# Optimization experiments

Measured on AMD Instinct MI355X. Metric: run time of the kernel, lower is better.

## Reference

```python
import jax, jax.numpy as jnp
import numpy as np

N_HEAD = 12
D_HEAD = 64


def setup_inputs() -> dict:
    key = jax.random.key(0)
    ks = jax.random.split(key, 9)
    bs, seq, d_model = 4, 2048, 768
    sc = 1.0 / np.sqrt(d_model)
    return {
        "q": jax.random.normal(ks[0], (bs, seq, d_model), jnp.float32),
        "k": jax.random.normal(ks[1], (bs, seq, d_model), jnp.float32),
        "v": jax.random.normal(ks[2], (bs, seq, d_model), jnp.float32),
        "Wq": jax.random.normal(ks[3], (d_model, d_model), jnp.float32) * sc,
        "bq": jax.random.normal(ks[4], (d_model,), jnp.float32) * 0.01,
        "Wk": jax.random.normal(ks[5], (d_model, d_model), jnp.float32) * sc,
        "bk": jax.random.normal(ks[6], (d_model,), jnp.float32) * 0.01,
        "Wv": jax.random.normal(ks[7], (d_model, d_model), jnp.float32) * sc,
        "bv": jax.random.normal(ks[8], (d_model,), jnp.float32) * 0.01,
    }


def _split_heads(x):
    # [bs, seq, n_head*d_head] -> [bs, n_head, seq, d_head]
    bs, seq, _ = x.shape
    return x.reshape(bs, seq, N_HEAD, D_HEAD).transpose(0, 2, 1, 3)


def reference(q, k, v, Wq, bq, Wk, bk, Wv, bv):
    # Linear projections (torch Linear: x @ W.T + b)
    wq = _split_heads(q @ Wq.T + bq)
    wk = _split_heads(k @ Wk.T + bk)
    wv = _split_heads(v @ Wv.T + bv)
    # scale=False in defaults -> raw dot products, no mask, dropout is eval no-op
    scores = jnp.einsum("bhqd,bhkd->bhqk", wq, wk)  # [bs, h, S, S]
    probs = jax.nn.softmax(scores, axis=-1)
    attn_vec = jnp.einsum("bhqk,bhkd->bhqd", probs, wv)
    bs, _, seq, _ = attn_vec.shape
    # merge heads -> [bs, seq, n_head*d_head]
    return attn_vec.transpose(0, 2, 1, 3).reshape(bs, seq, N_HEAD * D_HEAD)
```

## Files before the change

kernel.cpp:

```cpp
#include <hip/hip_runtime.h>
#include <stdint.h>

typedef _Float16 half8  __attribute__((ext_vector_type(8)));
typedef _Float16 half4v __attribute__((ext_vector_type(4)));
typedef float    floatx4 __attribute__((ext_vector_type(4)));

#define LOG2E 1.44269504088896340736f

__device__ __forceinline__ void gl_lds16(const _Float16* g, _Float16* l) {
  __builtin_amdgcn_global_load_lds(
      (__attribute__((address_space(1))) void*)g,
      (__attribute__((address_space(3))) void*)l, 16, 0, 0);
}
__device__ __forceinline__ void gl_lds16f(const float* g, float* l) {
  __builtin_amdgcn_global_load_lds(
      (__attribute__((address_space(1))) void*)g,
      (__attribute__((address_space(3))) void*)l, 16, 0, 0);
}

__device__ __forceinline__ half4v pack4(float a, float b, float c, float d) {
  auto lo = __builtin_amdgcn_cvt_pkrtz(a, b);
  auto hi = __builtin_amdgcn_cvt_pkrtz(c, d);
  return half4v{static_cast<_Float16>(lo[0]), static_cast<_Float16>(lo[1]),
                static_cast<_Float16>(hi[0]), static_cast<_Float16>(hi[1])};
}
__device__ __forceinline__ half8 cvt8(floatx4 a, floatx4 b) {
  half4v lo = pack4(a[0], a[1], a[2], a[3]);
  half4v hi = pack4(b[0], b[1], b[2], b[3]);
  return __builtin_shufflevector(lo, hi, 0, 1, 2, 3, 4, 5, 6, 7);
}

struct CvtArgs {
  const float* src[3];
  _Float16*    dst[3];
};

__global__ void cvt_kernel(CvtArgs a) {
  const int z = blockIdx.y;
  const int i = (blockIdx.x * 256 + threadIdx.x) * 8;
  const float4* s = (const float4*)(a.src[z] + i);
  float4 v0 = s[0], v1 = s[1];
  half8 h = { (_Float16)v0.x, (_Float16)v0.y, (_Float16)v0.z, (_Float16)v0.w,
              (_Float16)v1.x, (_Float16)v1.y, (_Float16)v1.z, (_Float16)v1.w };
  *(half8*)(a.dst[z] + i) = h;
}

__device__ __forceinline__ void gemm_stage(const float* __restrict__ X,
                                           const _Float16* __restrict__ W,
                                           float* Asb, _Float16* Bsb,
                                           int m0, int n0, int k0, int tid) {
  #pragma unroll
  for (int i = 0; i < 4; ++i) {
    int G = i * 256 + tid;
    int r = G >> 3, gl = G & 7;
    int g = gl ^ (r & 7);
    gl_lds16f(X + (size_t)(m0 + r) * 768 + k0 + g * 4, Asb + G * 4);
  }
  #pragma unroll
  for (int i = 0; i < 2; ++i) {
    int G = i * 256 + tid;
    int r = G >> 2, gl = G & 3;
    int g = gl ^ ((r >> 1) & 3);
    gl_lds16(W + (size_t)(n0 + r) * 768 + k0 + g * 8, Bsb + G * 8);
  }
}

template <int BUF>
__device__ __forceinline__ void gemm_body(
    int knext, const float* __restrict__ X, const _Float16* __restrict__ W,
    float* As, _Float16* Bs, int m0, int n0, int tid, int z,
    int wr, int wc, int qd, int col, floatx4 (&acc)[4][4])
{
  if (knext < 768)
    gemm_stage(X, W, As + (1 - BUF) * 4096, Bs + (1 - BUF) * 4096, m0, n0, knext, tid);

  half8 af[4], bf[4];
  #pragma unroll
  for (int t = 0; t < 4; ++t) {
    int ra = wr * 64 + t * 16 + col;
    const float* Ab = As + BUF * 4096 + ra * 32;
    floatx4 a0 = *(const floatx4*)(Ab + (((2 * qd)     ^ (ra & 7)) * 4));
    floatx4 a1 = *(const floatx4*)(Ab + (((2 * qd + 1) ^ (ra & 7)) * 4));
    af[t] = cvt8(a0, a1);
  }
  #pragma unroll
  for (int t = 0; t < 4; ++t) {
    int rb = wc * 64 + t * 16 + col;
    bf[t] = *(const half8*)(Bs + BUF * 4096 + rb * 32 + ((qd ^ ((rb >> 1) & 3)) * 8));
  }
  if (z == 2) {
    #pragma unroll
    for (int i = 0; i < 4; ++i)
      #pragma unroll
      for (int j = 0; j < 4; ++j)
        acc[i][j] = __builtin_amdgcn_mfma_f32_16x16x32_f16(af[i], bf[j], acc[i][j], 0, 0, 0);
  } else {
    #pragma unroll
    for (int i = 0; i < 4; ++i)
      #pragma unroll
      for (int j = 0; j < 4; ++j)
        acc[i][j] = __builtin_amdgcn_mfma_f32_16x16x32_f16(bf[j], af[i], acc[i][j], 0, 0, 0);
  }
  __syncthreads();
}

__global__ __launch_bounds__(256, 2) void qkv_gemm(
    const float* __restrict__ qx, const float* __restrict__ kx, const float* __restrict__ vx,
    const _Float16* __restrict__ wh,
    const float* __restrict__ bqp, const float* __restrict__ bkp, const float* __restrict__ bvp,
    _Float16* __restrict__ oq, _Float16* __restrict__ ok, _Float16* __restrict__ ovt)
{
  __shared__ __attribute__((aligned(16))) char smem[49152];
  float*    As = (float*)smem;
  _Float16* Bs = (_Float16*)(smem + 32768);
  _Float16* Es = (_Float16*)smem;

  const int z  = blockIdx.z;
  const float* X = (z == 0) ? qx : ((z == 1) ? kx : vx);
  const _Float16* W = wh + (size_t)z * 589824;
  const int m0 = blockIdx.x * 128, n0 = blockIdx.y * 128;
  const int tid  = threadIdx.x;
  const int lane = tid & 63, wid = tid >> 6;
  const int wr = wid >> 1, wc = wid & 1;
  const int qd = lane >> 4, col = lane & 15;

  const floatx4 z4 = {0.f, 0.f, 0.f, 0.f};
  floatx4 acc[4][4];
  #pragma unroll
  for (int i = 0; i < 4; ++i)
    #pragma unroll
    for (int j = 0; j < 4; ++j) acc[i][j] = z4;

  gemm_stage(X, W, As, Bs, m0, n0, 0, tid);
  __syncthreads();
  for (int kk = 0; kk < 768; kk += 64) {
    gemm_body<0>(kk + 32, X, W, As, Bs, m0, n0, tid, z, wr, wc, qd, col, acc);
    gemm_body<1>(kk + 64, X, W, As, Bs, m0, n0, tid, z, wr, wc, qd, col, acc);
  }

  const float* bias = (z == 0) ? bqp : ((z == 1) ? bkp : bvp);
  const int b = m0 >> 11, s0 = m0 & 2047;
  if (z == 2) {
    #pragma unroll
    for (int j = 0; j < 4; ++j) {
      int n_loc = wc * 64 + j * 16 + col;
      float bb = bias[n0 + n_loc];
      #pragma unroll
      for (int i = 0; i < 4; ++i) {
        int s_loc = wr * 64 + i * 16 + qd * 4;
        half4v h = pack4(acc[i][j][0] + bb, acc[i][j][1] + bb,
                         acc[i][j][2] + bb, acc[i][j][3] + bb);
        *(half4v*)(Es + n_loc * 160 + s_loc) = h;
      }
    }
    __syncthreads();
    #pragma unroll
    for (int it = 0; it < 8; ++it) {
      int row = it * 16 + (tid >> 4);
      int k   = tid & 15;
      half8 vr = *(const half8*)(Es + row * 160 + k * 8);
      *(half8*)(ovt + ((size_t)(b * 768 + n0 + row)) * 2048 + s0 + k * 8) = vr;
    }
  } else {
    _Float16* O = (z == 0) ? oq : ok;
    const float scale = (z == 0) ? LOG2E : 1.0f;
    #pragma unroll
    for (int j = 0; j < 4; ++j) {
      int n_loc = wc * 64 + j * 16 + qd * 4;
      float4 bb = *(const float4*)(bias + n0 + n_loc);
      #pragma unroll
      for (int i = 0; i < 4; ++i) {
        int s_loc = wr * 64 + i * 16 + col;
        half4v h = pack4((acc[i][j][0] + bb.x) * scale, (acc[i][j][1] + bb.y) * scale,
                         (acc[i][j][2] + bb.z) * scale, (acc[i][j][3] + bb.w) * scale);
        *(half4v*)(Es + s_loc * 160 + n_loc) = h;
      }
    }
    __syncthreads();
    const int hh0 = n0 >> 6;
    #pragma unroll
    for (int it = 0; it < 8; ++it) {
      int seg = it * 32 + (tid >> 3);
      int s = seg >> 1, hseg = seg & 1;
      int k = tid & 7;
      half8 vr = *(const half8*)(Es + s * 160 + hseg * 64 + k * 8);
      int mb = (m0 + s) >> 11, sg = (m0 + s) & 2047;
      *(half8*)(O + (size_t)(mb * 12 + hh0 + hseg) * 131072
                  + (size_t)sg * 64 + k * 8) = vr;
    }
  }
}


__device__ __forceinline__ void stage_issue(const _Float16* kp, const _Float16* vp,
                                            _Float16* ksd, int4 (&vr)[2], int tid) {
  #pragma unroll
  for (int i = 0; i < 2; ++i)
    gl_lds16(kp + i * 2048, ksd + (i * 256 + tid) * 8);
  #pragma unroll
  for (int i = 0; i < 2; ++i)
    vr[i] = *(const int4*)(vp + (size_t)i * 65536);
}

__device__ __forceinline__ void stage_write(char* vsd, int vwA, int vwB,
                                            const int4 (&vr)[2]) {
  #pragma unroll
  for (int i = 0; i < 2; ++i) {
    int2 lo; lo.x = vr[i].x; lo.y = vr[i].y;
    int2 hi; hi.x = vr[i].z; hi.y = vr[i].w;
    *(int2*)(vsd + vwA + i * 4096) = lo;
    *(int2*)(vsd + vwB + i * 4096) = hi;
  }
}

template <int BUF>
__device__ __forceinline__ void attn_body(
    bool pref, const _Float16*& kp, const _Float16*& vp,
    _Float16* Ks, char* Vs, int tid, int vwA, int vwB,
    const half8 (&qf)[2][2], int kb0, int kb1, const int (&vb)[4],
    float (&nm)[2], floatx4 (&ol)[2], floatx4 (&o)[4][2])
{
  int4 vr[2];
  if (pref) {
    stage_issue(kp, vp, Ks + (1 - BUF) * 4096, vr, tid);
    kp += 4096;
    vp += 64;
  }

  const char* ksb = (const char*)Ks + BUF * 8192;
  const char* vsb = Vs + BUF * 8192;

  half8 kf0[4], kf1[4];
  #pragma unroll
  for (int t = 0; t < 4; ++t) {
    kf0[t] = *(const half8*)(ksb + t * 2048 + kb0);
    kf1[t] = *(const half8*)(ksb + t * 2048 + kb1);
  }

  half4v pf[4][2];
  #pragma unroll
  for (int qt = 0; qt < 2; ++qt) {
    floatx4 seed = {nm[qt], nm[qt], nm[qt], nm[qt]};
    floatx4 st[4];
    #pragma unroll
    for (int t = 0; t < 4; ++t) {
      st[t] = __builtin_amdgcn_mfma_f32_16x16x32_f16(kf0[t], qf[qt][0], seed, 0, 0, 0);
      st[t] = __builtin_amdgcn_mfma_f32_16x16x32_f16(kf1[t], qf[qt][1], st[t], 0, 0, 0);
    }
    float v = fmaxf(
        fmaxf(fmaxf(fmaxf(st[0][0], st[0][1]), fmaxf(st[0][2], st[0][3])),
              fmaxf(fmaxf(st[1][0], st[1][1]), fmaxf(st[1][2], st[1][3]))),
        fmaxf(fmaxf(fmaxf(st[2][0], st[2][1]), fmaxf(st[2][2], st[2][3])),
              fmaxf(fmaxf(st[3][0], st[3][1]), fmaxf(st[3][2], st[3][3]))));
    v = fmaxf(v, __shfl_xor(v, 16, 64));
    v = fmaxf(v, __shfl_xor(v, 32, 64));
    if (__any(v > 0.f)) {
      float mr = fmaxf(v, 0.f);
      float al = __builtin_amdgcn_exp2f(-mr);
      nm[qt] -= mr;
      ol[qt] *= al;
      #pragma unroll
      for (int dt = 0; dt < 4; ++dt) o[dt][qt] *= al;
      #pragma unroll
      for (int t = 0; t < 4; ++t)
        pf[t][qt] = pack4(__builtin_amdgcn_exp2f(st[t][0] - mr),
                          __builtin_amdgcn_exp2f(st[t][1] - mr),
                          __builtin_amdgcn_exp2f(st[t][2] - mr),
                          __builtin_amdgcn_exp2f(st[t][3] - mr));
    } else {
      #pragma unroll
      for (int t = 0; t < 4; ++t)
        pf[t][qt] = pack4(__builtin_amdgcn_exp2f(st[t][0]),
                          __builtin_amdgcn_exp2f(st[t][1]),
                          __builtin_amdgcn_exp2f(st[t][2]),
                          __builtin_amdgcn_exp2f(st[t][3]));
    }
  }

  if (pref)
    stage_write(Vs + (1 - BUF) * 8192, vwA, vwB, vr);

  const half4v vone = {(_Float16)1.0f, (_Float16)1.0f, (_Float16)1.0f, (_Float16)1.0f};
  #pragma unroll
  for (int dt = 0; dt < 4; ++dt) {
    #pragma unroll
    for (int t = 0; t < 4; ++t) {
      half4v vf = *(const half4v*)(vsb + dt * 2048 + vb[t]);
      #pragma unroll
      for (int qt = 0; qt < 2; ++qt)
        o[dt][qt] = __builtin_amdgcn_mfma_f32_16x16x16f16(vf, pf[t][qt], o[dt][qt], 0, 0, 0);
    }
  }
  #pragma unroll
  for (int t = 0; t < 4; ++t)
    #pragma unroll
    for (int qt = 0; qt < 2; ++qt)
      ol[qt] = __builtin_amdgcn_mfma_f32_16x16x16f16(vone, pf[t][qt], ol[qt], 0, 0, 0);

  __syncthreads();
}

__global__ __launch_bounds__(256, 3) void attn_kernel(
    const _Float16* __restrict__ Qm,
    const _Float16* __restrict__ Km,
    const _Float16* __restrict__ Vt,
    float* __restrict__ out)
{
  __shared__ __attribute__((aligned(16))) _Float16 Ks[2 * 4096];
  __shared__ __attribute__((aligned(16))) char     Vs[2 * 8192];
  const int bh = blockIdx.x;
  const int q0 = blockIdx.y * 128;
  const int tid = threadIdx.x, lane = tid & 63, w = tid >> 6;
  const int qd = lane >> 4, col = lane & 15, c7 = col & 7;
  const _Float16* Qg = Qm + (size_t)bh * 131072;
  const _Float16* Kg = Km + (size_t)bh * 131072;
  const _Float16* Vg = Vt + (size_t)bh * 131072;

  half8 qf[2][2];
  #pragma unroll
  for (int qt = 0; qt < 2; ++qt)
    #pragma unroll
    for (int ks = 0; ks < 2; ++ks)
      qf[qt][ks] = *(const half8*)(Qg + (size_t)(q0 + w * 32 + qt * 16 + col) * 64
                                   + (ks * 4 + qd) * 8);

  const int kb0 = col * 128 + ((qd ^ c7) * 16);
  const int kb1 = col * 128 + (((4 + qd) ^ c7) * 16);
  const int rsz = ((col >> 3) ^ col) & 1;
  int vb[4];
  #pragma unroll
  for (int t = 0; t < 4; ++t)
    vb[t] = col * 128 + ((((2 * t) | (qd >> 1)) ^ c7) * 16) + (((qd & 1) ^ rsz) * 8);

  const int r0v = tid >> 3, scg = tid & 7;
  const int gsw = scg ^ (r0v & 7);
  const int wsz = ((r0v >> 3) ^ r0v) & 1;
  const int vwA = r0v * 128 + gsw * 16 + wsz * 8;
  const int vwB = vwA ^ 8;
  const _Float16* kp = Kg + r0v * 64 + gsw * 8;
  const _Float16* vp = Vg + (size_t)r0v * 2048 + scg * 8;

  float nm[2] = {100.f, 100.f};
  const floatx4 z4 = {0.f, 0.f, 0.f, 0.f};
  floatx4 ol[2] = {z4, z4};
  floatx4 o[4][2];
  #pragma unroll
  for (int dt = 0; dt < 4; ++dt)
    #pragma unroll
    for (int qt = 0; qt < 2; ++qt) o[dt][qt] = z4;

  {
    int4 vr0[2];
    stage_issue(kp, vp, Ks, vr0, tid);
    kp += 4096; vp += 64;
    stage_write(Vs, vwA, vwB, vr0);
  }
  __syncthreads();

  for (int jj = 0; jj < 2048; jj += 128) {
    attn_body<0>(true,            kp, vp, Ks, Vs, tid, vwA, vwB, qf, kb0, kb1, vb, nm, ol, o);
    attn_body<1>(jj + 128 < 2048, kp, vp, Ks, Vs, tid, vwA, vwB, qf, kb0, kb1, vb, nm, ol, o);
  }

  const int b = bh / 12, h = bh % 12;
  #pragma unroll
  for (int qt = 0; qt < 2; ++qt) {
    float inv = 1.0f / ol[qt][0];
    int qg = q0 + w * 32 + qt * 16 + col;
    float* obase = out + ((size_t)b * 2048 + qg) * 768 + h * 64;
    #pragma unroll
    for (int dt = 0; dt < 4; ++dt) {
      floatx4 v = o[dt][qt];
      v *= inv;
      *(floatx4*)(obase + dt * 16 + qd * 4) = v;
    }
  }
}

extern "C" void kernel_launch(void* const* d_in, const int* in_sizes, int n_in,
                              void* d_out, int out_size, void* d_ws, size_t ws_size,
                              hipStream_t stream) {
  const float* q  = (const float*)d_in[0];
  const float* k  = (const float*)d_in[1];
  const float* v  = (const float*)d_in[2];
  const float* Wq = (const float*)d_in[3];
  const float* bq = (const float*)d_in[4];
  const float* Wk = (const float*)d_in[5];
  const float* bk = (const float*)d_in[6];
  const float* Wv = (const float*)d_in[7];
  const float* bv = (const float*)d_in[8];

  const size_t NX = 6291456;
  const size_t NW = 589824;
  const size_t need = (3 * NW + 3 * NX) * sizeof(_Float16);
  if (ws_size < need) return;

  _Float16* wh = (_Float16*)d_ws;
  _Float16* qh = wh + 3 * NW;
  _Float16* kh = qh + NX;
  _Float16* vt = kh + NX;

  CvtArgs ca;
  ca.src[0] = Wq; ca.src[1] = Wk; ca.src[2] = Wv;
  ca.dst[0] = wh; ca.dst[1] = wh + NW; ca.dst[2] = wh + 2 * NW;

  cvt_kernel<<<dim3(288, 3), 256, 0, stream>>>(ca);
  qkv_gemm<<<dim3(64, 6, 3), 256, 0, stream>>>(q, k, v, wh, bq, bk, bv, qh, kh, vt);
  attn_kernel<<<dim3(48, 16), 256, 0, stream>>>(qh, kh, vt, (float*)d_out);
}
```

Before: 258.5 us.

## Triple-buffer K/V in LDS with async direct loads and vmcnt-based barriers

Moves K/V staging from a double buffer to a three-stage ring. V now goes straight to LDS through global_load_lds instead of passing through registers, with a new XOR swizzle for its reads. Each step waits on vmcnt, issues a single barrier and then prefetches two tiles ahead, which removes the trailing __syncthreads and the register round trip for V. It also raises wave priority around the MFMA blocks with s_setprio. The costs are more LDS per block, which may limit occupancy, and a hand-counted vmcnt schedule that must exactly cover all 32 tiles.

```diff
diff --git a/kernel.cpp b/kernel.cpp
--- a/kernel.cpp
+++ b/kernel.cpp
@@ -192,44 +192,23 @@
 }
 
 
-__device__ __forceinline__ void stage_issue(const _Float16* kp, const _Float16* vp,
-                                            _Float16* ksd, int4 (&vr)[2], int tid) {
-  #pragma unroll
-  for (int i = 0; i < 2; ++i)
-    gl_lds16(kp + i * 2048, ksd + (i * 256 + tid) * 8);
-  #pragma unroll
-  for (int i = 0; i < 2; ++i)
-    vr[i] = *(const int4*)(vp + (size_t)i * 65536);
-}
-
-__device__ __forceinline__ void stage_write(char* vsd, int vwA, int vwB,
-                                            const int4 (&vr)[2]) {
+__device__ __forceinline__ void stage_kv(const _Float16* __restrict__ Kg,
+                                         const _Float16* __restrict__ Vg,
+                                         _Float16* ksd, _Float16* vsd, int j0, int tid) {
   #pragma unroll
   for (int i = 0; i < 2; ++i) {
-    int2 lo; lo.x = vr[i].x; lo.y = vr[i].y;
-    int2 hi; hi.x = vr[i].z; hi.y = vr[i].w;
-    *(int2*)(vsd + vwA + i * 4096) = lo;
-    *(int2*)(vsd + vwB + i * 4096) = hi;
-  }
-}
-
-template <int BUF>
-__device__ __forceinline__ void attn_body(
-    bool pref, const _Float16*& kp, const _Float16*& vp,
-    _Float16* Ks, char* Vs, int tid, int vwA, int vwB,
+    int c = i * 256 + tid;
+    int row = c >> 3, sc = c & 7;
+    gl_lds16(Kg + (size_t)(j0 + row) * 64 + ((sc ^ (row & 7)) * 8), ksd + c * 8);
+    gl_lds16(Vg + (size_t)row * 2048 + j0 + ((sc ^ (row & 7)) * 8), vsd + c * 8);
+  }
+}
+
+__device__ __forceinline__ void attn_half(
+    const char* ksb, const char* vsb,
     const half8 (&qf)[2][2], int kb0, int kb1, const int (&vb)[4],
     float (&nm)[2], floatx4 (&ol)[2], floatx4 (&o)[4][2])
 {
-  int4 vr[2];
-  if (pref) {
-    stage_issue(kp, vp, Ks + (1 - BUF) * 4096, vr, tid);
-    kp += 4096;
-    vp += 64;
-  }
-
-  const char* ksb = (const char*)Ks + BUF * 8192;
-  const char* vsb = Vs + BUF * 8192;
-
   half8 kf0[4], kf1[4];
   #pragma unroll
   for (int t = 0; t < 4; ++t) {
@@ -242,11 +221,13 @@
   for (int qt = 0; qt < 2; ++qt) {
     floatx4 seed = {nm[qt], nm[qt], nm[qt], nm[qt]};
     floatx4 st[4];
+    __builtin_amdgcn_s_setprio(1);
     #pragma unroll
     for (int t = 0; t < 4; ++t) {
       st[t] = __builtin_amdgcn_mfma_f32_16x16x32_f16(kf0[t], qf[qt][0], seed, 0, 0, 0);
       st[t] = __builtin_amdgcn_mfma_f32_16x16x32_f16(kf1[t], qf[qt][1], st[t], 0, 0, 0);
     }
+    __builtin_amdgcn_s_setprio(0);
     float v = fmaxf(
         fmaxf(fmaxf(fmaxf(st[0][0], st[0][1]), fmaxf(st[0][2], st[0][3])),
               fmaxf(fmaxf(st[1][0], st[1][1]), fmaxf(st[1][2], st[1][3]))),
@@ -277,10 +258,8 @@
     }
   }
 
-  if (pref)
-    stage_write(Vs + (1 - BUF) * 8192, vwA, vwB, vr);
-
   const half4v vone = {(_Float16)1.0f, (_Float16)1.0f, (_Float16)1.0f, (_Float16)1.0f};
+  __builtin_amdgcn_s_setprio(1);
   #pragma unroll
   for (int dt = 0; dt < 4; ++dt) {
     #pragma unroll
@@ -296,8 +275,24 @@
     #pragma unroll
     for (int qt = 0; qt < 2; ++qt)
       ol[qt] = __builtin_amdgcn_mfma_f32_16x16x16f16(vone, pf[t][qt], ol[qt], 0, 0, 0);
-
-  __syncthreads();
+  __builtin_amdgcn_s_setprio(0);
+}
+
+template <int RB, int WB, int VM>
+__device__ __forceinline__ void attn_body(
+    bool pref, int jn, const _Float16* __restrict__ Kg, const _Float16* __restrict__ Vg,
+    _Float16* Ks, _Float16* Vs, int tid,
+    const half8 (&qf)[2][2], int kb0, int kb1, const int (&vb)[4],
+    float (&nm)[2], floatx4 (&ol)[2], floatx4 (&o)[4][2])
+{
+  asm volatile("s_waitcnt vmcnt(%0)" :: "i"(VM) : "memory");
+  __builtin_amdgcn_s_barrier();
+  __builtin_amdgcn_sched_barrier(0);
+  if (pref)
+    stage_kv(Kg, Vg, Ks + WB * 4096, Vs + WB * 4096, jn, tid);
+  __builtin_amdgcn_sched_barrier(0);
+  attn_half((const char*)(Ks + RB * 4096), (const char*)(Vs + RB * 4096),
+            qf, kb0, kb1, vb, nm, ol, o);
 }
 
 __global__ __launch_bounds__(256, 3) void attn_kernel(
@@ -306,8 +301,8 @@
     const _Float16* __restrict__ Vt,
     float* __restrict__ out)
 {
-  __shared__ __attribute__((aligned(16))) _Float16 Ks[2 * 4096];
-  __shared__ __attribute__((aligned(16))) char     Vs[2 * 8192];
+  __shared__ __attribute__((aligned(16))) _Float16 Ks[3 * 4096];
+  __shared__ __attribute__((aligned(16))) _Float16 Vs[3 * 4096];
   const int bh = blockIdx.x;
   const int q0 = blockIdx.y * 128;
   const int tid = threadIdx.x, lane = tid & 63, w = tid >> 6;
@@ -326,19 +321,11 @@
 
   const int kb0 = col * 128 + ((qd ^ c7) * 16);
   const int kb1 = col * 128 + (((4 + qd) ^ c7) * 16);
-  const int rsz = ((col >> 3) ^ col) & 1;
+  const int vq = (qd >> 1) ^ c7;
   int vb[4];
   #pragma unroll
   for (int t = 0; t < 4; ++t)
-    vb[t] = col * 128 + ((((2 * t) | (qd >> 1)) ^ c7) * 16) + (((qd & 1) ^ rsz) * 8);
-
-  const int r0v = tid >> 3, scg = tid & 7;
-  const int gsw = scg ^ (r0v & 7);
-  const int wsz = ((r0v >> 3) ^ r0v) & 1;
-  const int vwA = r0v * 128 + gsw * 16 + wsz * 8;
-  const int vwB = vwA ^ 8;
-  const _Float16* kp = Kg + r0v * 64 + gsw * 8;
-  const _Float16* vp = Vg + (size_t)r0v * 2048 + scg * 8;
+    vb[t] = col * 128 + (qd & 1) * 8 + ((vq ^ (2 * t)) * 16);
 
   float nm[2] = {100.f, 100.f};
   const floatx4 z4 = {0.f, 0.f, 0.f, 0.f};
@@ -349,18 +336,19 @@
     #pragma unroll
     for (int qt = 0; qt < 2; ++qt) o[dt][qt] = z4;
 
-  {
-    int4 vr0[2];
-    stage_issue(kp, vp, Ks, vr0, tid);
-    kp += 4096; vp += 64;
-    stage_write(Vs, vwA, vwB, vr0);
-  }
-  __syncthreads();
-
-  for (int jj = 0; jj < 2048; jj += 128) {
-    attn_body<0>(true,            kp, vp, Ks, Vs, tid, vwA, vwB, qf, kb0, kb1, vb, nm, ol, o);
-    attn_body<1>(jj + 128 < 2048, kp, vp, Ks, Vs, tid, vwA, vwB, qf, kb0, kb1, vb, nm, ol, o);
-  }
+  stage_kv(Kg, Vg, Ks,        Vs,        0,  tid);
+  stage_kv(Kg, Vg, Ks + 4096, Vs + 4096, 64, tid);
+
+  int jn = 128;
+  #pragma unroll 1
+  for (int it = 0; it < 10; ++it) {
+    attn_body<0, 2, 4>(true, jn,       Kg, Vg, Ks, Vs, tid, qf, kb0, kb1, vb, nm, ol, o);
+    attn_body<1, 0, 4>(true, jn + 64,  Kg, Vg, Ks, Vs, tid, qf, kb0, kb1, vb, nm, ol, o);
+    attn_body<2, 1, 4>(true, jn + 128, Kg, Vg, Ks, Vs, tid, qf, kb0, kb1, vb, nm, ol, o);
+    jn += 192;
+  }
+  attn_body<0, 2, 4>(false, 0, Kg, Vg, Ks, Vs, tid, qf, kb0, kb1, vb, nm, ol, o);
+  attn_body<1, 0, 0>(false, 0, Kg, Vg, Ks, Vs, tid, qf, kb0, kb1, vb, nm, ol, o);
 
   const int b = bh / 12, h = bh % 12;
   #pragma unroll
```

After: 258.4 us. Within noise of the previous version (-0.0%).
